# Optimization experiments

Hardware: AMD Instinct MI355X
Metric: run time of the kernel (lower is better)

The kernel has to match this reference:

```python
import jax, jax.numpy as jnp
import numpy as np

B, FEAT, FIELD, K = 16384, 2048, 32, 64

def setup_inputs() -> dict:
    key = jax.random.key(0)
    k1, k2, k3, k4 = jax.random.split(key, 4)
    x = jax.random.normal(k1, (B, FEAT), dtype=jnp.float32)
    # nn.Linear(feature_size, 1): weight [1, FEAT] (use vector), bias [1] (scalar)
    w = jax.random.normal(k2, (FEAT,), dtype=jnp.float32) / np.sqrt(FEAT)
    b = jax.random.normal(k3, (), dtype=jnp.float32)
    # v ~ N(0, 0.01) as in torch.normal(0, 0.01, ...)
    v = 0.01 * jax.random.normal(k4, (FEAT, FIELD, K), dtype=jnp.float32)
    return {"x": x, "w": w, "b": b, "v": v}

def reference(x, w, b, v):
    # linear part: Linear(feature_size, 1).squeeze() -> [B]
    linear_part = x @ w + b  # [B]
    # field_x = tensordot(x, v, dims=1) -> [B, FIELD, K]
    field_x = jnp.einsum('bf,fsk->bsk', x, v)
    # sum_{i<j} sum_k f_i * f_j  ==  0.5 * (||sum_i f_i||^2 - sum_i ||f_i||^2)
    s = field_x.sum(axis=1)                      # [B, K]
    sq = (field_x * field_x).sum(axis=(1, 2))    # [B]
    interaction = 0.5 * ((s * s).sum(axis=-1) - sq)  # [B]
    return jax.nn.sigmoid(linear_part + interaction)
```

## Files before the change

kernel.cpp:

```cpp
#include <hip/hip_runtime.h>
#include <cstdint>
#include <cstddef>

#define B_ROWS 16384
#define FEAT   2048
#define FIELD  32
#define KDIM   64
#define NCOLS  2048
#define NAUG   2176

using half8   = __attribute__((ext_vector_type(8))) _Float16;
using half4   = __attribute__((ext_vector_type(4))) _Float16;
using floatx4 = __attribute__((ext_vector_type(4))) float;

__device__ __forceinline__ void load_lds16(const void* g, void* l) {
  __builtin_amdgcn_global_load_lds((const __attribute__((address_space(1))) void*)g,
                                   (__attribute__((address_space(3))) void*)l, 16, 0, 0);
}

__global__ __launch_bounds__(256) void k_prep(const float* __restrict__ x,
                                              const float* __restrict__ v,
                                              const float* __restrict__ w,
                                              _Float16* __restrict__ xh,
                                              _Float16* __restrict__ vt,
                                              float* __restrict__ arg) {
  const int bb = blockIdx.x;
  const int t = threadIdx.x;
  if (bb < 8192) {
    size_t i = ((size_t)bb * 256 + t) * 16;
    float4 v0 = *(const float4*)(x + i);
    float4 v1 = *(const float4*)(x + i + 4);
    float4 v2 = *(const float4*)(x + i + 8);
    float4 v3 = *(const float4*)(x + i + 12);
    half8 h0 = { (_Float16)v0.x, (_Float16)v0.y, (_Float16)v0.z, (_Float16)v0.w,
                 (_Float16)v1.x, (_Float16)v1.y, (_Float16)v1.z, (_Float16)v1.w };
    half8 h1 = { (_Float16)v2.x, (_Float16)v2.y, (_Float16)v2.z, (_Float16)v2.w,
                 (_Float16)v3.x, (_Float16)v3.y, (_Float16)v3.z, (_Float16)v3.w };
    *(half8*)(xh + i) = h0;
    *(half8*)(xh + i + 8) = h1;
  } else if (bb < 9216) {
    __shared__ _Float16 tile[64 * 68];
    const int b2 = bb - 8192;
    const int f0 = (b2 >> 5) * 64;
    const int n0 = (b2 & 31) * 64;
#pragma unroll
    for (int j = 0; j < 4; ++j) {
      int c = j * 256 + t;
      int row = c >> 4;
      int col = (c & 15) * 4;
      float4 val = *(const float4*)(v + (size_t)(f0 + row) * NCOLS + n0 + col);
      tile[row * 68 + col + 0] = (_Float16)val.x;
      tile[row * 68 + col + 1] = (_Float16)val.y;
      tile[row * 68 + col + 2] = (_Float16)val.z;
      tile[row * 68 + col + 3] = (_Float16)val.w;
    }
    __syncthreads();
#pragma unroll
    for (int j = 0; j < 4; ++j) {
      int c = j * 256 + t;
      int nl = c >> 4;
      int fl = (c & 15) * 4;
      half4 h = { tile[(fl + 0) * 68 + nl], tile[(fl + 1) * 68 + nl],
                  tile[(fl + 2) * 68 + nl], tile[(fl + 3) * 68 + nl] };
      *(half4*)(vt + (size_t)(n0 + nl) * FEAT + f0 + fl) = h;
    }
  } else if (bb < 9728) {
    const int k = t & 63;
    const int f = (bb - 9216) * 4 + (t >> 6);
    float s = 0.f;
#pragma unroll
    for (int si = 0; si < FIELD; ++si) s += v[(size_t)f * NCOLS + si * KDIM + k];
    vt[(size_t)(NCOLS + k) * FEAT + f] = (_Float16)s;
  } else if (bb < 10240) {
    int idx = (bb - 9728) * 256 + t;
    int r = NCOLS + KDIM + (idx >> 11);
    int f = idx & 2047;
    vt[(size_t)r * FEAT + f] = (r == NCOLS + KDIM) ? (_Float16)w[f] : (_Float16)0.f;
  } else {
    arg[(bb - 10240) * 256 + t] = 0.f;
  }
}

__global__ __launch_bounds__(256) void k_gemm(const _Float16* __restrict__ xh,
                                              const _Float16* __restrict__ vt,
                                              float* __restrict__ arg) {
  __shared__ __align__(16) _Float16 lds_a[128 * 64];
  __shared__ __align__(16) _Float16 lds_b[128 * 64];
  const int t = threadIdx.x;
  const int m0 = blockIdx.x * 128;
  const int n0 = blockIdx.y * 128;
  const int lane = t & 63;
  const int wave = t >> 6;
  const int wm = (wave & 1) * 64;
  const int wn = (wave >> 1) * 64;
  const int lr = lane & 15;
  const int lk = (lane >> 4) * 8;

  floatx4 acc[4][4] = {};

  for (int k0 = 0; k0 < FEAT; k0 += 64) {
#pragma unroll
    for (int i = 0; i < 4; ++i) {
      int c = i * 256 + t;
      int row = c >> 3;
      int g = (c & 7) ^ (row & 7);
      load_lds16(xh + (size_t)(m0 + row) * FEAT + k0 + g * 8, lds_a + c * 8);
      load_lds16(vt + (size_t)(n0 + row) * FEAT + k0 + g * 8, lds_b + c * 8);
    }
    __syncthreads();
#pragma unroll
    for (int ks = 0; ks < 64; ks += 32) {
      const int kc = (ks + lk) >> 3;
      half8 af[4], bf[4];
#pragma unroll
      for (int f = 0; f < 4; ++f) {
        int ma = wm + f * 16 + lr;
        int nb = wn + f * 16 + lr;
        af[f] = *(const half8*)(lds_a + ma * 64 + (kc ^ (ma & 7)) * 8);
        bf[f] = *(const half8*)(lds_b + nb * 64 + (kc ^ (nb & 7)) * 8);
      }
#pragma unroll
      for (int fm = 0; fm < 4; ++fm)
#pragma unroll
        for (int fn = 0; fn < 4; ++fn)
          acc[fm][fn] = __builtin_amdgcn_mfma_f32_16x16x32_f16(af[fm], bf[fn],
                                                               acc[fm][fn], 0, 0, 0);
    }
    __syncthreads();
  }

  const int cq = lane >> 4;
#pragma unroll
  for (int fm = 0; fm < 4; ++fm) {
#pragma unroll
    for (int r = 0; r < 4; ++r) {
      float contrib = 0.f;
#pragma unroll
      for (int fn = 0; fn < 4; ++fn) {
        int col = n0 + wn + fn * 16 + lr;
        float vv = acc[fm][fn][r];
        float q = vv * vv;
        if (col < NCOLS)                contrib -= 0.5f * q;
        else if (col < NCOLS + KDIM)    contrib += 0.5f * q;
        else if (col == NCOLS + KDIM)   contrib += vv;
      }
      contrib += __shfl_xor(contrib, 1);
      contrib += __shfl_xor(contrib, 2);
      contrib += __shfl_xor(contrib, 4);
      contrib += __shfl_xor(contrib, 8);
      if (lr == 0) atomicAdd(&arg[m0 + wm + fm * 16 + cq * 4 + r], contrib);
    }
  }
}

__global__ __launch_bounds__(256) void k_fin(const float* __restrict__ arg,
                                             const float* __restrict__ b,
                                             float* __restrict__ out) {
  int i = blockIdx.x * 256 + threadIdx.x;
  float z = arg[i] + b[0];
  out[i] = 1.f / (1.f + __expf(-z));
}

extern "C" void kernel_launch(void* const* d_in, const int* in_sizes, int n_in,
                              void* d_out, int out_size, void* d_ws, size_t ws_size,
                              hipStream_t stream) {
  const float* x = (const float*)d_in[0];
  const float* w = (const float*)d_in[1];
  const float* b = (const float*)d_in[2];
  const float* v = (const float*)d_in[3];
  float* out = (float*)d_out;

  char* ws = (char*)d_ws;
  _Float16* xh  = (_Float16*)ws;
  _Float16* vt  = (_Float16*)(ws + 67108864);
  float*    arg = (float*)(ws + 67108864 + 8912896);

  k_prep<<<10304, 256, 0, stream>>>(x, v, w, xh, vt, arg);
  k_gemm<<<dim3(128, 17), 256, 0, stream>>>(xh, vt, arg);
  k_fin<<<64, 256, 0, stream>>>(arg, b, out);
}
```

Before: 422.3 us.

## Rewrite GEMM as 256x256-tile, 8-wave, multi-buffered pipelined kernel

The GEMM kernel moves from 128x128 tiles with 4 waves and a single LDS buffer to 256x256 tiles with 8 waves. LDS is now split into multiple buffers so global-to-LDS loads for later k-steps are issued while MFMAs run on the current one, with explicit vmcnt/lgkmcnt waits, barriers, sched_barrier and setprio. Block IDs are remapped into an XCD-aware order, and out-of-range B rows are clamped. The aim is to hide memory latency and raise data reuse per block. In exchange it uses 128 KB of LDS per block and the N tiles (2176 columns) leave more padded work per tile.

```diff
diff --git a/kernel.cpp b/kernel.cpp
--- a/kernel.cpp
+++ b/kernel.cpp
@@ -81,74 +81,166 @@
   }
 }
 
-__global__ __launch_bounds__(256) void k_gemm(const _Float16* __restrict__ xh,
-                                              const _Float16* __restrict__ vt,
-                                              float* __restrict__ arg) {
-  __shared__ __align__(16) _Float16 lds_a[128 * 64];
-  __shared__ __align__(16) _Float16 lds_b[128 * 64];
-  const int t = threadIdx.x;
-  const int m0 = blockIdx.x * 128;
-  const int n0 = blockIdx.y * 128;
-  const int lane = t & 63;
-  const int wave = t >> 6;
-  const int wm = (wave & 1) * 64;
-  const int wn = (wave >> 1) * 64;
-  const int lr = lane & 15;
-  const int lk = (lane >> 4) * 8;
-
-  floatx4 acc[4][4] = {};
-
-  for (int k0 = 0; k0 < FEAT; k0 += 64) {
-#pragma unroll
-    for (int i = 0; i < 4; ++i) {
-      int c = i * 256 + t;
-      int row = c >> 3;
-      int g = (c & 7) ^ (row & 7);
-      load_lds16(xh + (size_t)(m0 + row) * FEAT + k0 + g * 8, lds_a + c * 8);
-      load_lds16(vt + (size_t)(n0 + row) * FEAT + k0 + g * 8, lds_b + c * 8);
-    }
-    __syncthreads();
-#pragma unroll
-    for (int ks = 0; ks < 64; ks += 32) {
-      const int kc = (ks + lk) >> 3;
-      half8 af[4], bf[4];
-#pragma unroll
-      for (int f = 0; f < 4; ++f) {
-        int ma = wm + f * 16 + lr;
-        int nb = wn + f * 16 + lr;
-        af[f] = *(const half8*)(lds_a + ma * 64 + (kc ^ (ma & 7)) * 8);
-        bf[f] = *(const half8*)(lds_b + nb * 64 + (kc ^ (nb & 7)) * 8);
-      }
-#pragma unroll
-      for (int fm = 0; fm < 4; ++fm)
-#pragma unroll
-        for (int fn = 0; fn < 4; ++fn)
-          acc[fm][fn] = __builtin_amdgcn_mfma_f32_16x16x32_f16(af[fm], bf[fn],
-                                                               acc[fm][fn], 0, 0, 0);
-    }
-    __syncthreads();
-  }
+__global__ __launch_bounds__(512, 2) void k_gemm(const _Float16* __restrict__ xh,
+                                                 const _Float16* __restrict__ vt,
+                                                 float* __restrict__ arg) {
+  __shared__ __align__(16) _Float16 lds[65536];
+  const int tid  = threadIdx.x;
+  const int lane = tid & 63;
+  const int wave = tid >> 6;
+  const int wm   = wave >> 2;
+  const int wn   = wave & 3;
+  const int lr   = lane & 15;
+  const int q    = lane >> 4;
+
+  const int bid = blockIdx.x;
+  const int wg  = (bid & 7) * 72 + (bid >> 3);
+  const int m0  = (wg & 63) * 256;
+  const int n0  = (wg >> 6) * 256;
+
+  int offA[4], offB[4];
+#pragma unroll
+  for (int f = 0; f < 4; ++f) {
+    int L = f * 16 + lr;
+    int u = wm * 4 + q;
+    offA[f] = L * 64 + ((u ^ (L & 7)) * 8);
+  }
+#pragma unroll
+  for (int g = 0; g < 4; ++g) {
+    int L = (wn & 1) * 64 + g * 16 + lr;
+    int u = (wn >> 1) * 4 + q;
+    offB[g] = L * 64 + ((u ^ (L & 7)) * 8);
+  }
+
+  const int L0   = tid >> 3;
+  const int u0   = (tid & 7) ^ (L0 & 7);
+  const int row0 = (u0 >> 2) * 128 + L0;
+  const int kc0  = u0 & 3;
+  const _Float16* pA0 = xh + (size_t)(m0 + row0) * FEAT + kc0 * 8;
+  const _Float16* pA1 = pA0 + (size_t)64 * FEAT;
+  const int rb0 = (n0 + row0      < NAUG) ? n0 + row0      : NAUG - 1;
+  const int rb1 = (n0 + row0 + 64 < NAUG) ? n0 + row0 + 64 : NAUG - 1;
+  const _Float16* pB0 = vt + (size_t)rb0 * FEAT + kc0 * 8;
+  const _Float16* pB1 = vt + (size_t)rb1 * FEAT + kc0 * 8;
+
+  auto stageA = [&](int koff, int seg) {
+    load_lds16(pA0 + koff, lds + seg + tid * 8);
+    load_lds16(pA1 + koff, lds + seg + 4096 + tid * 8);
+  };
+  auto stageB = [&](int koff, int seg) {
+    load_lds16(pB0 + koff, lds + seg + tid * 8);
+    load_lds16(pB1 + koff, lds + seg + 4096 + tid * 8);
+  };
+
+  floatx4 acc[8][4] = {};
+  half8 af[4], bf[4];
+
+  stageA(0, 0);       stageB(0, 32768);
+  stageA(32, 8192);   stageB(32, 40960);
+  stageA(64, 16384);  stageB(64, 49152);
+  asm volatile("s_waitcnt vmcnt(4)" ::: "memory");
+  __builtin_amdgcn_s_barrier();
+
+#define PHASE_TAIL()                                        \
+    __builtin_amdgcn_s_barrier();                           \
+    asm volatile("s_waitcnt lgkmcnt(0)" ::: "memory");      \
+    __builtin_amdgcn_sched_barrier(0);                      \
+    __builtin_amdgcn_s_setprio(1)
+
+#define PHASE_END()                                         \
+    __builtin_amdgcn_s_setprio(0);                          \
+    __builtin_amdgcn_s_barrier()
+
+#pragma unroll 2
+  for (int t = 0; t < 32; ++t) {
+    const int sA0  = ((t & 1) << 1) * 8192;
+    const int sB0  = 32768 + sA0;
+    const int sPA1 = ((((t + 1) & 1) << 1) | 1) * 8192;
+
+#pragma unroll
+    for (int g = 0; g < 4; ++g) bf[g] = *(const half8*)(lds + sB0 + offB[g]);
+#pragma unroll
+    for (int f = 0; f < 4; ++f) af[f] = *(const half8*)(lds + sA0 + offA[f]);
+    if (t < 31) stageA((t + 1) * 64 + 32, sPA1);
+    PHASE_TAIL();
+#pragma unroll
+    for (int f = 0; f < 4; ++f)
+#pragma unroll
+      for (int g = 0; g < 4; ++g)
+        acc[f][g] = __builtin_amdgcn_mfma_f32_16x16x32_f16(af[f], bf[g],
+                                                           acc[f][g], 0, 0, 0);
+    PHASE_END();
+
+#pragma unroll
+    for (int f = 0; f < 4; ++f) af[f] = *(const half8*)(lds + sA0 + 4096 + offA[f]);
+    if (t < 31) stageB((t + 1) * 64 + 32, 32768 + sPA1);
+    PHASE_TAIL();
+#pragma unroll
+    for (int f = 0; f < 4; ++f)
+#pragma unroll
+      for (int g = 0; g < 4; ++g)
+        acc[4 + f][g] = __builtin_amdgcn_mfma_f32_16x16x32_f16(af[f], bf[g],
+                                                               acc[4 + f][g], 0, 0, 0);
+    PHASE_END();
+
+#pragma unroll
+    for (int g = 0; g < 4; ++g) bf[g] = *(const half8*)(lds + sB0 + 8192 + offB[g]);
+#pragma unroll
+    for (int f = 0; f < 4; ++f) af[f] = *(const half8*)(lds + sA0 + 8192 + offA[f]);
+    if (t < 30) stageA((t + 2) * 64, sA0);
+    PHASE_TAIL();
+#pragma unroll
+    for (int f = 0; f < 4; ++f)
+#pragma unroll
+      for (int g = 0; g < 4; ++g)
+        acc[f][g] = __builtin_amdgcn_mfma_f32_16x16x32_f16(af[f], bf[g],
+                                                           acc[f][g], 0, 0, 0);
+    PHASE_END();
+
+#pragma unroll
+    for (int f = 0; f < 4; ++f) af[f] = *(const half8*)(lds + sA0 + 12288 + offA[f]);
+    if (t < 30) stageB((t + 2) * 64, sB0);
+    __builtin_amdgcn_s_barrier();
+    asm volatile("s_waitcnt lgkmcnt(0)" ::: "memory");
+    __builtin_amdgcn_sched_barrier(0);
+    __builtin_amdgcn_s_setprio(1);
+#pragma unroll
+    for (int f = 0; f < 4; ++f)
+#pragma unroll
+      for (int g = 0; g < 4; ++g)
+        acc[4 + f][g] = __builtin_amdgcn_mfma_f32_16x16x32_f16(af[f], bf[g],
+                                                               acc[4 + f][g], 0, 0, 0);
+    __builtin_amdgcn_s_setprio(0);
+    if (t < 30) { asm volatile("s_waitcnt vmcnt(4)" ::: "memory"); }
+    else        { asm volatile("s_waitcnt vmcnt(0)" ::: "memory"); }
+    __builtin_amdgcn_sched_barrier(0);
+    __builtin_amdgcn_s_barrier();
+  }
+#undef PHASE_TAIL
+#undef PHASE_END
 
   const int cq = lane >> 4;
-#pragma unroll
-  for (int fm = 0; fm < 4; ++fm) {
+  const int mrow = m0 + wm * 128;
+  const int ncol = n0 + wn * 64;
+#pragma unroll
+  for (int f = 0; f < 8; ++f) {
 #pragma unroll
     for (int r = 0; r < 4; ++r) {
       float contrib = 0.f;
 #pragma unroll
-      for (int fn = 0; fn < 4; ++fn) {
-        int col = n0 + wn + fn * 16 + lr;
-        float vv = acc[fm][fn][r];
-        float q = vv * vv;
-        if (col < NCOLS)                contrib -= 0.5f * q;
-        else if (col < NCOLS + KDIM)    contrib += 0.5f * q;
+      for (int g = 0; g < 4; ++g) {
+        int col = ncol + g * 16 + lr;
+        float vv = acc[f][g][r];
+        float qv = vv * vv;
+        if (col < NCOLS)                contrib -= 0.5f * qv;
+        else if (col < NCOLS + KDIM)    contrib += 0.5f * qv;
         else if (col == NCOLS + KDIM)   contrib += vv;
       }
       contrib += __shfl_xor(contrib, 1);
       contrib += __shfl_xor(contrib, 2);
       contrib += __shfl_xor(contrib, 4);
       contrib += __shfl_xor(contrib, 8);
-      if (lr == 0) atomicAdd(&arg[m0 + wm + fm * 16 + cq * 4 + r], contrib);
+      if (lr == 0) atomicAdd(&arg[mrow + f * 16 + cq * 4 + r], contrib);
     }
   }
 }
@@ -176,6 +268,6 @@
   float*    arg = (float*)(ws + 67108864 + 8912896);
 
   k_prep<<<10304, 256, 0, stream>>>(x, v, w, xh, vt, arg);
-  k_gemm<<<dim3(128, 17), 256, 0, stream>>>(xh, vt, arg);
+  k_gemm<<<576, 512, 0, stream>>>(xh, vt, arg);
   k_fin<<<64, 256, 0, stream>>>(arg, b, out);
 }
```

Result: faster. 394.4 us (-6.6%).
